# Performance work log

Hardware: AMD Instinct MI355X
Metric: run time of the kernel (lower is better)

The kernel has to match this reference:

```python
import jax, jax.numpy as jnp
import numpy as np

LEAKY_SLOPE = 0.01  # torch F.leaky_relu default


def _l2norm(x):
    # matches F.normalize(p=2, dim=-1, eps=1e-12)
    n = jnp.linalg.norm(x, axis=-1, keepdims=True)
    return x / jnp.maximum(n, 1e-12)


def setup_inputs() -> dict:
    key = jax.random.key(0)
    k1, k2, k3, k4 = jax.random.split(key, 4)
    B, S, H = 16, 256, 768
    return {
        "query_embs": jax.random.normal(k1, (B, S, H), dtype=jnp.float32),
        "key_embs": jax.random.normal(k2, (2 * B, S, H), dtype=jnp.float32),
        "logit_scale": jnp.log(jnp.asarray(1.0 / 0.07, dtype=jnp.float32)),
        "alpha_raw": jnp.asarray(1.0, dtype=jnp.float32),
        "q_mask": jax.random.randint(k3, (B, S), 0, 2).astype(jnp.int32),
        "k_mask": jax.random.randint(k4, (2 * B, S), 0, 2).astype(jnp.int32),
    }


def reference(query_embs, key_embs, logit_scale, alpha_raw, q_mask, k_mask):
    q = _l2norm(query_embs)                 # [B, S, H]
    k = _l2norm(key_embs)                   # [2B, S, H]
    S = q.shape[1]

    # all-pairs token similarity: [B, 2B, S, S]
    sim = jnp.einsum('ish,jth->ijst', q, k)

    # exponential distance weighting
    pos = jnp.arange(S)
    dist = jnp.abs(pos[:, None] - pos[None, :]).astype(sim.dtype)
    alpha = jax.nn.leaky_relu(alpha_raw, LEAKY_SLOPE)
    sim = sim * jnp.exp(-alpha * dist)

    # joint validity mask: q_mask[i,s] & k_mask[j,t]
    valid = (q_mask[:, None, :, None] * k_mask[None, :, None, :]) > 0

    logits = jnp.where(valid, jnp.exp(logit_scale) * sim, -jnp.inf)
    p = jnp.nan_to_num(jax.nn.softmax(logits, axis=-1), nan=0.0)  # fully-masked rows -> 0

    # softmax-weighted aggregation of key tokens, then dot with query tokens
    agg = jnp.einsum('ijst,jth->ijsh', p, k)        # [B, 2B, S, H]
    per_tok = jnp.einsum('ish,ijsh->ijs', q, agg)   # [B, 2B, S]
    per_tok = per_tok * q_mask[:, None, :].astype(per_tok.dtype)
    return per_tok.sum(axis=-1)                     # [B, 2B]
```

## Files before the change

### kernel.cpp

```cpp
#include <hip/hip_runtime.h>
#include <hip/hip_bf16.h>

#define BQ   16
#define BK2  32
#define SEQ  256
#define HD   768

typedef __attribute__((ext_vector_type(8))) short bf16x8;
typedef __attribute__((ext_vector_type(4))) float f32x4;

__device__ __forceinline__ void glds16(const unsigned short* g, unsigned short* l) {
    __builtin_amdgcn_global_load_lds(
        (const __attribute__((address_space(1))) unsigned int*)g,
        (__attribute__((address_space(3))) unsigned int*)l, 16, 0, 0);
}

__device__ __forceinline__ unsigned int pack2_bf16(float a, float b) {
    unsigned ua = __float_as_uint(a), ub = __float_as_uint(b);
    ua += 0x7FFFu + ((ua >> 16) & 1u);
    ub += 0x7FFFu + ((ub >> 16) & 1u);
    return (ua >> 16) | (ub & 0xFFFF0000u);
}

__global__ __launch_bounds__(256) void norm_kernel(
    const float* __restrict__ q, const float* __restrict__ k,
    unsigned short* __restrict__ qn, unsigned short* __restrict__ kn,
    float* __restrict__ out)
{
    if (blockIdx.x == 0 && threadIdx.x < 256) {
        out[threadIdx.x] = 0.f; out[threadIdx.x + 256] = 0.f;
    }
    int row  = blockIdx.x * 4 + (threadIdx.x >> 6);
    int lane = threadIdx.x & 63;
    const int NQ = BQ * SEQ;
    const float* src = (row < NQ) ? q + (size_t)row * HD
                                  : k + (size_t)(row - NQ) * HD;
    unsigned int* dst = (unsigned int*)((row < NQ) ? qn + (size_t)row * HD
                                                   : kn + (size_t)(row - NQ) * HD);
    float4 v[3];
    float ss = 0.f;
#pragma unroll
    for (int c = 0; c < 3; ++c) {
        v[c] = ((const float4*)src)[lane + 64 * c];
        ss += v[c].x * v[c].x + v[c].y * v[c].y + v[c].z * v[c].z + v[c].w * v[c].w;
    }
#pragma unroll
    for (int m = 1; m < 64; m <<= 1) ss += __shfl_xor(ss, m, 64);
    float inv = rsqrtf(fmaxf(ss, 1e-24f));
#pragma unroll
    for (int c = 0; c < 3; ++c) {
        uint2 o = make_uint2(pack2_bf16(v[c].x * inv, v[c].y * inv),
                             pack2_bf16(v[c].z * inv, v[c].w * inv));
        ((uint2*)dst)[lane + 64 * c] = o;
    }
}

__global__ __launch_bounds__(256, 4) void li_kernel(
    const unsigned short* __restrict__ qn, const unsigned short* __restrict__ kn,
    const float* __restrict__ g_ls, const float* __restrict__ g_ar,
    const int* __restrict__ q_mask, const int* __restrict__ k_mask,
    float* __restrict__ out)
{
    const int j  = blockIdx.x, i = blockIdx.y, sh = blockIdx.z;
    const int tid  = threadIdx.x;
    const int w    = tid >> 6, lane = tid & 63;
    const int ln   = lane & 15, lg = lane >> 4;
    const int wt   = w;

    __shared__ __align__(16) unsigned short As[64 * 64];
    __shared__ __align__(16) unsigned short Bs[256 * 64];

    float a0 = g_ar[0];
    float alpha = (a0 > 0.f) ? a0 : 0.01f * a0;
    float scale = __expf(g_ls[0]);

    const int rl  = lane >> 3;
    const int gch = (lane & 7) ^ rl;
    const unsigned short* aq = qn + ((size_t)i * SEQ + sh * 64 + w * 8 + rl) * HD + gch * 8;
    const unsigned short* bq = kn + ((size_t)j * SEQ + w * 8 + rl) * HD + gch * 8;
    unsigned short* al = As + (w * 8) * 64;
    unsigned short* bl = Bs + (w * 8) * 64;

    f32x4 acc[4][4];
    const f32x4 zero4 = {0.f, 0.f, 0.f, 0.f};
#pragma unroll
    for (int a = 0; a < 4; ++a)
#pragma unroll
        for (int b = 0; b < 4; ++b) acc[a][b] = zero4;

    for (int kk = 0; kk < HD; kk += 64) {
        __syncthreads();
#pragma unroll
        for (int c = 0; c < 2; ++c)
            glds16(aq + kk + c * (32 * HD), al + c * (32 * 64));
#pragma unroll
        for (int c = 0; c < 8; ++c)
            glds16(bq + kk + c * (32 * HD), bl + c * (32 * 64));
        __syncthreads();
        const bf16x8* A8 = (const bf16x8*)As;
        const bf16x8* B8 = (const bf16x8*)Bs;
#pragma unroll
        for (int ks = 0; ks < 2; ++ks) {
            const int ch = (ks * 4 + lg) ^ (ln & 7);
            bf16x8 af[4], bfr[4];
#pragma unroll
            for (int rm = 0; rm < 4; ++rm)
                af[rm] = A8[(rm * 16 + ln) * 8 + ch];
#pragma unroll
            for (int cn = 0; cn < 4; ++cn)
                bfr[cn] = B8[(wt * 64 + cn * 16 + ln) * 8 + ch];
#pragma unroll
            for (int rm = 0; rm < 4; ++rm)
#pragma unroll
                for (int cn = 0; cn < 4; ++cn)
                    acc[rm][cn] = __builtin_amdgcn_mfma_f32_16x16x32_bf16(
                        af[rm], bfr[cn], acc[rm][cn], 0, 0, 0);
        }
    }

    float kmv[4];
#pragma unroll
    for (int cn = 0; cn < 4; ++cn)
        kmv[cn] = (k_mask[j * SEQ + wt * 64 + cn * 16 + ln] != 0) ? 1.f : 0.f;

    __syncthreads();
    float* zs  = (float*)As;
    float* wsc = zs + 256;

#pragma unroll
    for (int rm = 0; rm < 4; ++rm)
#pragma unroll
        for (int r = 0; r < 4; ++r) {
            int srow = rm * 16 + lg * 4 + r;
            int s  = sh * 64 + srow;
            float ze = 0.f, we = 0.f;
#pragma unroll
            for (int cn = 0; cn < 4; ++cn) {
                int t = wt * 64 + cn * 16 + ln;
                float sim = acc[rm][cn][r];
                int d = s - t; d = (d < 0) ? -d : d;
                float wd = __expf(-alpha * (float)d);
                float e  = kmv[cn] * __expf(sim * scale * wd);
                ze += e;
                we = fmaf(e, sim, we);
            }
#pragma unroll
            for (int m = 1; m < 16; m <<= 1) {
                ze += __shfl_xor(ze, m, 64);
                we += __shfl_xor(we, m, 64);
            }
            if (ln == 0) { zs[srow * 4 + wt] = ze; wsc[srow * 4 + wt] = we; }
        }
    __syncthreads();

    if (w == 0) {
        const float4 Z4 = ((const float4*)zs)[lane];
        const float4 W4 = ((const float4*)wsc)[lane];
        float Z = Z4.x + Z4.y + Z4.z + Z4.w;
        float W = W4.x + W4.y + W4.z + W4.w;
        float pt = (Z > 0.f) ? (W / Z) : 0.f;
        float part = pt * (float)q_mask[i * SEQ + sh * 64 + lane];
#pragma unroll
        for (int m = 1; m < 64; m <<= 1) part += __shfl_xor(part, m, 64);
        if (lane == 0) atomicAdd(&out[i * BK2 + j], part);
    }
}

extern "C" void kernel_launch(void* const* d_in, const int* in_sizes, int n_in,
                              void* d_out, int out_size, void* d_ws, size_t ws_size,
                              hipStream_t stream) {
    const float* q  = (const float*)d_in[0];
    const float* k  = (const float*)d_in[1];
    const float* ls = (const float*)d_in[2];
    const float* ar = (const float*)d_in[3];
    const int* qm   = (const int*)d_in[4];
    const int* km   = (const int*)d_in[5];
    float* out      = (float*)d_out;

    unsigned short* qn = (unsigned short*)d_ws;
    unsigned short* kn = qn + (size_t)BQ * SEQ * HD;

    norm_kernel<<<(BQ + BK2) * SEQ / 4, 256, 0, stream>>>(q, k, qn, kn, (float*)d_out);
    li_kernel<<<dim3(BK2, BQ, 4), 256, 0, stream>>>(qn, kn, ls, ar, qm, km, (float*)d_out);
}
```

Baseline: 150.9 us.

## Fuse normalization and similarity kernels into one cooperative persistent kernel

Merges the L2-normalization kernel and the attention-style similarity kernel into a single cooperative launch. A grid-wide sync separates the two phases, and blocks loop persistently over row and tile work units. The aim is to remove the second launch and the gap between kernels. In exchange it adds a host occupancy query, grid-sync overhead and a persistent loop that may reduce occupancy or load balance.

```diff
diff --git a/kernel.cpp b/kernel.cpp
--- a/kernel.cpp
+++ b/kernel.cpp
@@ -1,10 +1,15 @@
 #include <hip/hip_runtime.h>
 #include <hip/hip_bf16.h>
+#include <hip/hip_cooperative_groups.h>
+
+namespace cg = cooperative_groups;
 
 #define BQ   16
 #define BK2  32
 #define SEQ  256
 #define HD   768
+#define NROWS ((BQ + BK2) * SEQ)
+#define NUNITS (BQ * BK2 * 4)
 
 typedef __attribute__((ext_vector_type(8))) short bf16x8;
 typedef __attribute__((ext_vector_type(4))) float f32x4;
@@ -22,53 +27,48 @@
     return (ua >> 16) | (ub & 0xFFFF0000u);
 }
 
-__global__ __launch_bounds__(256) void norm_kernel(
+__global__ __launch_bounds__(256, 4) void fused_kernel(
     const float* __restrict__ q, const float* __restrict__ k,
-    unsigned short* __restrict__ qn, unsigned short* __restrict__ kn,
-    float* __restrict__ out)
-{
-    if (blockIdx.x == 0 && threadIdx.x < 256) {
-        out[threadIdx.x] = 0.f; out[threadIdx.x + 256] = 0.f;
-    }
-    int row  = blockIdx.x * 4 + (threadIdx.x >> 6);
-    int lane = threadIdx.x & 63;
-    const int NQ = BQ * SEQ;
-    const float* src = (row < NQ) ? q + (size_t)row * HD
-                                  : k + (size_t)(row - NQ) * HD;
-    unsigned int* dst = (unsigned int*)((row < NQ) ? qn + (size_t)row * HD
-                                                   : kn + (size_t)(row - NQ) * HD);
-    float4 v[3];
-    float ss = 0.f;
-#pragma unroll
-    for (int c = 0; c < 3; ++c) {
-        v[c] = ((const float4*)src)[lane + 64 * c];
-        ss += v[c].x * v[c].x + v[c].y * v[c].y + v[c].z * v[c].z + v[c].w * v[c].w;
-    }
-#pragma unroll
-    for (int m = 1; m < 64; m <<= 1) ss += __shfl_xor(ss, m, 64);
-    float inv = rsqrtf(fmaxf(ss, 1e-24f));
-#pragma unroll
-    for (int c = 0; c < 3; ++c) {
-        uint2 o = make_uint2(pack2_bf16(v[c].x * inv, v[c].y * inv),
-                             pack2_bf16(v[c].z * inv, v[c].w * inv));
-        ((uint2*)dst)[lane + 64 * c] = o;
-    }
-}
-
-__global__ __launch_bounds__(256, 4) void li_kernel(
-    const unsigned short* __restrict__ qn, const unsigned short* __restrict__ kn,
     const float* __restrict__ g_ls, const float* __restrict__ g_ar,
     const int* __restrict__ q_mask, const int* __restrict__ k_mask,
-    float* __restrict__ out)
+    unsigned short* __restrict__ qn, unsigned short* __restrict__ kn,
+    float* __restrict__ out, int nblocks)
 {
-    const int j  = blockIdx.x, i = blockIdx.y, sh = blockIdx.z;
+    const int bid  = blockIdx.x;
     const int tid  = threadIdx.x;
     const int w    = tid >> 6, lane = tid & 63;
     const int ln   = lane & 15, lg = lane >> 4;
-    const int wt   = w;
 
     __shared__ __align__(16) unsigned short As[64 * 64];
     __shared__ __align__(16) unsigned short Bs[256 * 64];
+
+    if (bid == 0) { out[tid] = 0.f; out[tid + 256] = 0.f; }
+    const int nwaves = nblocks * 4;
+    for (int row = bid * 4 + w; row < NROWS; row += nwaves) {
+        const float* src = (row < BQ * SEQ) ? q + (size_t)row * HD
+                                            : k + (size_t)(row - BQ * SEQ) * HD;
+        unsigned int* dst = (unsigned int*)((row < BQ * SEQ)
+                              ? qn + (size_t)row * HD
+                              : kn + (size_t)(row - BQ * SEQ) * HD);
+        float4 v[3];
+        float ss = 0.f;
+#pragma unroll
+        for (int c = 0; c < 3; ++c) {
+            v[c] = ((const float4*)src)[lane + 64 * c];
+            ss += v[c].x * v[c].x + v[c].y * v[c].y + v[c].z * v[c].z + v[c].w * v[c].w;
+        }
+#pragma unroll
+        for (int m = 1; m < 64; m <<= 1) ss += __shfl_xor(ss, m, 64);
+        float inv = rsqrtf(fmaxf(ss, 1e-24f));
+#pragma unroll
+        for (int c = 0; c < 3; ++c) {
+            uint2 o = make_uint2(pack2_bf16(v[c].x * inv, v[c].y * inv),
+                                 pack2_bf16(v[c].z * inv, v[c].w * inv));
+            ((uint2*)dst)[lane + 64 * c] = o;
+        }
+    }
+
+    cg::this_grid().sync();
 
     float a0 = g_ar[0];
     float alpha = (a0 > 0.f) ? a0 : 0.01f * a0;
@@ -76,93 +76,98 @@
 
     const int rl  = lane >> 3;
     const int gch = (lane & 7) ^ rl;
-    const unsigned short* aq = qn + ((size_t)i * SEQ + sh * 64 + w * 8 + rl) * HD + gch * 8;
-    const unsigned short* bq = kn + ((size_t)j * SEQ + w * 8 + rl) * HD + gch * 8;
-    unsigned short* al = As + (w * 8) * 64;
-    unsigned short* bl = Bs + (w * 8) * 64;
 
-    f32x4 acc[4][4];
-    const f32x4 zero4 = {0.f, 0.f, 0.f, 0.f};
+    for (int unit = bid; unit < NUNITS; unit += nblocks) {
+        const int sh = unit & 3, j = (unit >> 2) & 31, i = unit >> 7;
+
+        const unsigned short* aq = qn + ((size_t)i * SEQ + sh * 64 + w * 8 + rl) * HD + gch * 8;
+        const unsigned short* bq = kn + ((size_t)j * SEQ + w * 8 + rl) * HD + gch * 8;
+        unsigned short* al = As + (w * 8) * 64;
+        unsigned short* bl = Bs + (w * 8) * 64;
+
+        f32x4 acc[4][4];
+        const f32x4 zero4 = {0.f, 0.f, 0.f, 0.f};
 #pragma unroll
-    for (int a = 0; a < 4; ++a)
+        for (int a = 0; a < 4; ++a)
 #pragma unroll
-        for (int b = 0; b < 4; ++b) acc[a][b] = zero4;
+            for (int b = 0; b < 4; ++b) acc[a][b] = zero4;
 
-    for (int kk = 0; kk < HD; kk += 64) {
-        __syncthreads();
+        for (int kk = 0; kk < HD; kk += 64) {
+            __syncthreads();
 #pragma unroll
-        for (int c = 0; c < 2; ++c)
-            glds16(aq + kk + c * (32 * HD), al + c * (32 * 64));
+            for (int c = 0; c < 2; ++c)
+                glds16(aq + kk + c * (32 * HD), al + c * (32 * 64));
 #pragma unroll
-        for (int c = 0; c < 8; ++c)
-            glds16(bq + kk + c * (32 * HD), bl + c * (32 * 64));
-        __syncthreads();
-        const bf16x8* A8 = (const bf16x8*)As;
-        const bf16x8* B8 = (const bf16x8*)Bs;
+            for (int c = 0; c < 8; ++c)
+                glds16(bq + kk + c * (32 * HD), bl + c * (32 * 64));
+            __syncthreads();
+            const bf16x8* A8 = (const bf16x8*)As;
+            const bf16x8* B8 = (const bf16x8*)Bs;
 #pragma unroll
-        for (int ks = 0; ks < 2; ++ks) {
-            const int ch = (ks * 4 + lg) ^ (ln & 7);
-            bf16x8 af[4], bfr[4];
+            for (int ks = 0; ks < 2; ++ks) {
+                const int ch = (ks * 4 + lg) ^ (ln & 7);
+                bf16x8 af[4], bfr[4];
 #pragma unroll
-            for (int rm = 0; rm < 4; ++rm)
-                af[rm] = A8[(rm * 16 + ln) * 8 + ch];
-#pragma unroll
-            for (int cn = 0; cn < 4; ++cn)
-                bfr[cn] = B8[(wt * 64 + cn * 16 + ln) * 8 + ch];
-#pragma unroll
-            for (int rm = 0; rm < 4; ++rm)
+                for (int rm = 0; rm < 4; ++rm)
+                    af[rm] = A8[(rm * 16 + ln) * 8 + ch];
 #pragma unroll
                 for (int cn = 0; cn < 4; ++cn)
-                    acc[rm][cn] = __builtin_amdgcn_mfma_f32_16x16x32_bf16(
-                        af[rm], bfr[cn], acc[rm][cn], 0, 0, 0);
+                    bfr[cn] = B8[(w * 64 + cn * 16 + ln) * 8 + ch];
+#pragma unroll
+                for (int rm = 0; rm < 4; ++rm)
+#pragma unroll
+                    for (int cn = 0; cn < 4; ++cn)
+                        acc[rm][cn] = __builtin_amdgcn_mfma_f32_16x16x32_bf16(
+                            af[rm], bfr[cn], acc[rm][cn], 0, 0, 0);
+            }
         }
-    }
 
-    float kmv[4];
+        float kmv[4];
 #pragma unroll
-    for (int cn = 0; cn < 4; ++cn)
-        kmv[cn] = (k_mask[j * SEQ + wt * 64 + cn * 16 + ln] != 0) ? 1.f : 0.f;
+        for (int cn = 0; cn < 4; ++cn)
+            kmv[cn] = (k_mask[j * SEQ + w * 64 + cn * 16 + ln] != 0) ? 1.f : 0.f;
 
-    __syncthreads();
-    float* zs  = (float*)As;
-    float* wsc = zs + 256;
+        __syncthreads();
+        float* zs  = (float*)As;
+        float* wsc = zs + 256;
 
 #pragma unroll
-    for (int rm = 0; rm < 4; ++rm)
+        for (int rm = 0; rm < 4; ++rm)
 #pragma unroll
-        for (int r = 0; r < 4; ++r) {
-            int srow = rm * 16 + lg * 4 + r;
-            int s  = sh * 64 + srow;
-            float ze = 0.f, we = 0.f;
+            for (int r = 0; r < 4; ++r) {
+                int srow = rm * 16 + lg * 4 + r;
+                int s  = sh * 64 + srow;
+                float ze = 0.f, we = 0.f;
 #pragma unroll
-            for (int cn = 0; cn < 4; ++cn) {
-                int t = wt * 64 + cn * 16 + ln;
-                float sim = acc[rm][cn][r];
-                int d = s - t; d = (d < 0) ? -d : d;
-                float wd = __expf(-alpha * (float)d);
-                float e  = kmv[cn] * __expf(sim * scale * wd);
-                ze += e;
-                we = fmaf(e, sim, we);
+                for (int cn = 0; cn < 4; ++cn) {
+                    int t = w * 64 + cn * 16 + ln;
+                    float sim = acc[rm][cn][r];
+                    int d = s - t; d = (d < 0) ? -d : d;
+                    float wd = __expf(-alpha * (float)d);
+                    float e  = kmv[cn] * __expf(sim * scale * wd);
+                    ze += e;
+                    we = fmaf(e, sim, we);
+                }
+#pragma unroll
+                for (int m = 1; m < 16; m <<= 1) {
+                    ze += __shfl_xor(ze, m, 64);
+                    we += __shfl_xor(we, m, 64);
+                }
+                if (ln == 0) { zs[srow * 4 + w] = ze; wsc[srow * 4 + w] = we; }
             }
+        __syncthreads();
+
+        if (w == 0) {
+            const float4 Z4 = ((const float4*)zs)[lane];
+            const float4 W4 = ((const float4*)wsc)[lane];
+            float Z = Z4.x + Z4.y + Z4.z + Z4.w;
+            float W = W4.x + W4.y + W4.z + W4.w;
+            float pt = (Z > 0.f) ? (W / Z) : 0.f;
+            float part = pt * (float)q_mask[i * SEQ + sh * 64 + lane];
 #pragma unroll
-            for (int m = 1; m < 16; m <<= 1) {
-                ze += __shfl_xor(ze, m, 64);
-                we += __shfl_xor(we, m, 64);
-            }
-            if (ln == 0) { zs[srow * 4 + wt] = ze; wsc[srow * 4 + wt] = we; }
+            for (int m = 1; m < 64; m <<= 1) part += __shfl_xor(part, m, 64);
+            if (lane == 0) atomicAdd(&out[i * BK2 + j], part);
         }
-    __syncthreads();
-
-    if (w == 0) {
-        const float4 Z4 = ((const float4*)zs)[lane];
-        const float4 W4 = ((const float4*)wsc)[lane];
-        float Z = Z4.x + Z4.y + Z4.z + Z4.w;
-        float W = W4.x + W4.y + W4.z + W4.w;
-        float pt = (Z > 0.f) ? (W / Z) : 0.f;
-        float part = pt * (float)q_mask[i * SEQ + sh * 64 + lane];
-#pragma unroll
-        for (int m = 1; m < 64; m <<= 1) part += __shfl_xor(part, m, 64);
-        if (lane == 0) atomicAdd(&out[i * BK2 + j], part);
     }
 }
 
@@ -180,6 +185,15 @@
     unsigned short* qn = (unsigned short*)d_ws;
     unsigned short* kn = qn + (size_t)BQ * SEQ * HD;
 
-    norm_kernel<<<(BQ + BK2) * SEQ / 4, 256, 0, stream>>>(q, k, qn, kn, (float*)d_out);
-    li_kernel<<<dim3(BK2, BQ, 4), 256, 0, stream>>>(qn, kn, ls, ar, qm, km, (float*)d_out);
+    int bpc = 0;
+    hipOccupancyMaxActiveBlocksPerMultiprocessor(&bpc, fused_kernel, 256, 0);
+    if (bpc < 1) bpc = 1;
+    int nblocks = bpc * 256;
+    if (nblocks > NUNITS) nblocks = NUNITS;
+
+    void* args[] = {(void*)&q, (void*)&k, (void*)&ls, (void*)&ar,
+                    (void*)&qm, (void*)&km, (void*)&qn, (void*)&kn,
+                    (void*)&out, (void*)&nblocks};
+    hipLaunchCooperativeKernel((const void*)fused_kernel, dim3(nblocks),
+                               dim3(256), args, 0, stream);
 }
```

Measured after the change: 246.3 us. 1.63x slower.
